# Optimization experiments

Measured on AMD Instinct MI355X. Metric: run time of the kernel, lower is better.

The kernel has to match this reference:

```python
import jax, jax.numpy as jnp
import numpy as np

N, DIM, H, DH = 2048, 1024, 16, 64
LARGE_NEG = -1e10
LN_EPS = 1e-6  # flax LayerNorm default


def setup_inputs() -> dict:
    key = jax.random.key(0)
    ks = jax.random.split(key, 6)
    x = jax.random.normal(ks[0], (N, DIM), dtype=jnp.float32)
    pos_sin = jax.random.uniform(ks[1], (N - 1, DH // 2), dtype=jnp.float32)
    pos_cos = jax.random.uniform(ks[2], (N - 1, DH // 2), dtype=jnp.float32)
    mask = jax.random.bernoulli(ks[3], 0.9, (N - 1,))
    ln_scale = jnp.ones((DIM,), jnp.float32)
    ln_bias = jnp.zeros((DIM,), jnp.float32)
    w_qkv = jax.random.normal(ks[4], (DIM, 3 * H * DH), jnp.float32) * (DIM ** -0.5)
    w_out = jax.random.normal(ks[5], (H * DH, DIM), jnp.float32) * ((H * DH) ** -0.5)
    b_out = jnp.zeros((DIM,), jnp.float32)
    return {"x": x, "pos_sin": pos_sin, "pos_cos": pos_cos, "mask": mask,
            "ln_scale": ln_scale, "ln_bias": ln_bias,
            "w_qkv": w_qkv, "w_out": w_out, "b_out": b_out}


def _rotate_every_two(t):
    # t: [i, h, d] -> pairwise rotation along d
    x1 = t[:, :, ::2]
    x2 = t[:, :, 1::2]
    return jnp.stack((-x2, x1), axis=-1).reshape(t.shape)


def _apply_rope(t, sin, cos):
    # sin/cos: [i, d/2] -> interleave-repeat to [i, 1, d] (einops 'b n -> b (n j)', j=2)
    sin2 = jnp.repeat(sin, 2, axis=-1)[:, None, :]
    cos2 = jnp.repeat(cos, 2, axis=-1)[:, None, :]
    return t * cos2 + _rotate_every_two(t) * sin2


def reference(x, pos_sin, pos_cos, mask, ln_scale, ln_bias, w_qkv, w_out, b_out):
    n, dim_in = x.shape
    scale = dim_in ** -0.5  # NOTE: full model dim, as in the source

    # LayerNorm over last axis
    mu = jnp.mean(x, axis=-1, keepdims=True)
    var = jnp.mean(jnp.square(x - mu), axis=-1, keepdims=True)
    xn = (x - mu) * jax.lax.rsqrt(var + LN_EPS) * ln_scale + ln_bias

    # QKV projection (no bias)
    qkv = xn @ w_qkv  # [n, 3*h*d]
    q, k, v = jnp.split(qkv, 3, axis=-1)
    q, k, v = (t.reshape(n, H, DH) for t in (q, k, v))

    # Selective RoPE: rotate all positions except the first token
    q = q.at[1:].set(_apply_rope(q[1:], pos_sin, pos_cos))
    k = k.at[1:].set(_apply_rope(k[1:], pos_sin, pos_cos))

    # Head-last similarity [i, j, h]
    sim = jnp.einsum('ihd,jhd->ijh', q, k) * scale

    # Padding mask: prepend True for position 0, broadcast as (1, j, 1)
    pad_mask = jnp.pad(mask, (1, 0), constant_values=True)[None, :, None]

    # Causal mask: triu of an (n-1)x(n-1) block padded with False on row/col 0
    tri = jnp.pad(jnp.ones((n - 1, n - 1), bool), ((1, 0), (1, 0)), constant_values=False)
    causal_mask = jnp.triu(tri, 1)[:, :, None]  # k = j - i + 1 = 1
    full_mask = (~causal_mask) & pad_mask

    sim = jnp.where(full_mask, sim, LARGE_NEG)
    attn = jax.nn.softmax(sim, axis=-2)  # softmax over j (non-last axis)

    out = jnp.einsum('ijh,jhd->ihd', attn, v).reshape(n, H * DH)
    return out @ w_out + b_out
```

## Files before the change

### kernel.cpp

```cpp
#include <hip/hip_runtime.h>
#include <hip/hip_bf16.h>
#include <stdint.h>

typedef __bf16 bf16_t;
typedef __bf16 bf16x8 __attribute__((ext_vector_type(8)));
typedef __bf16 bf16x4 __attribute__((ext_vector_type(4)));
typedef float  f32x4  __attribute__((ext_vector_type(4)));

#define DEV __device__ __forceinline__

static constexpr int NTOK = 2048;
static constexpr int DIM  = 1024;
static constexpr int NH   = 16;
static constexpr int DH   = 64;
static constexpr int QKVN = 3072;
static constexpr int SLOTS_PER_HEAD = 40;
static constexpr int PART_SLOTS = 36;
static constexpr int PART_STRIDE = 17408;
static constexpr float L2E = 1.44269504f;

__device__ static constexpr unsigned char SLOT_ORDER[40] = {
    39, 38, 37, 36, 34, 33, 32, 30, 29, 28, 26, 25, 24, 23,
    22, 21, 19, 18, 16, 15, 13, 12, 11, 10, 8, 6, 4, 3,
    35, 20, 9, 2,
    31, 17, 7, 1,
    27, 14, 5, 0};

DEV void gload_lds16(const void* g, void* l) {
  __builtin_amdgcn_global_load_lds(
      (__attribute__((address_space(1))) void*)(g),
      (__attribute__((address_space(3))) void*)(l), 16, 0, 0);
}

DEV float bf2f(bf16_t b) { return (float)b; }

__global__ __launch_bounds__(256) void k_ln_tc(const float* __restrict__ x,
                                               const float* __restrict__ gamma,
                                               const float* __restrict__ beta,
                                               bf16_t* __restrict__ xn,
                                               const float* __restrict__ wsrc,
                                               bf16_t* __restrict__ wdst,
                                               const float* __restrict__ wosrc,
                                               bf16_t* __restrict__ wodst) {
  __shared__ float tile[64][65];
  __shared__ float red[8];
  int b = blockIdx.x;
  if (b < NTOK) {
    const int row = b;
    const int t = threadIdx.x;
    const float4* x4 = reinterpret_cast<const float4*>(x);
    float4 v = x4[(size_t)row * 256 + t];
    float s  = v.x + v.y + v.z + v.w;
    float s2 = v.x * v.x + v.y * v.y + v.z * v.z + v.w * v.w;
#pragma unroll
    for (int o = 1; o < 64; o <<= 1) {
      s  += __shfl_xor(s, o, 64);
      s2 += __shfl_xor(s2, o, 64);
    }
    const int w = t >> 6, lane = t & 63;
    if (lane == 0) { red[w] = s; red[4 + w] = s2; }
    __syncthreads();
    s  = red[0] + red[1] + red[2] + red[3];
    s2 = red[4] + red[5] + red[6] + red[7];
    const float mu  = s * (1.0f / 1024.0f);
    const float var = s2 * (1.0f / 1024.0f) - mu * mu;
    const float inv = rsqrtf(var + 1e-6f);
    const float4 g = reinterpret_cast<const float4*>(gamma)[t];
    const float4 bb = reinterpret_cast<const float4*>(beta)[t];
    bf16x4 o;
    o[0] = (bf16_t)((v.x - mu) * inv * g.x + bb.x);
    o[1] = (bf16_t)((v.y - mu) * inv * g.y + bb.y);
    o[2] = (bf16_t)((v.z - mu) * inv * g.z + bb.z);
    o[3] = (bf16_t)((v.w - mu) * inv * g.w + bb.w);
    *reinterpret_cast<bf16x4*>(xn + (size_t)row * DIM + t * 4) = o;
  } else if (b < NTOK + 768) {
    b -= NTOK;
    const int c0 = (b % 48) * 64;
    const int r0 = (b / 48) * 64;
    const int tx = threadIdx.x & 63;
    const int ty = threadIdx.x >> 6;
#pragma unroll
    for (int i = 0; i < 16; ++i) {
      int r = ty + i * 4;
      tile[r][tx] = wsrc[(size_t)(r0 + r) * 3072 + c0 + tx];
    }
    __syncthreads();
#pragma unroll
    for (int i = 0; i < 16; ++i) {
      int r = ty + i * 4;
      wdst[(size_t)(c0 + r) * 1024 + r0 + tx] = (bf16_t)tile[tx][r];
    }
  } else {
    b -= (NTOK + 768);
    const int c0 = (b & 15) * 64;
    const int r0 = (b >> 4) * 64;
    const int tx = threadIdx.x & 63;
    const int ty = threadIdx.x >> 6;
#pragma unroll
    for (int i = 0; i < 16; ++i) {
      int r = ty + i * 4;
      tile[r][tx] = wosrc[(size_t)(r0 + r) * 1024 + c0 + tx];
    }
    __syncthreads();
#pragma unroll
    for (int i = 0; i < 16; ++i) {
      int r = ty + i * 4;
      wodst[(size_t)(c0 + r) * 1024 + r0 + tx] = (bf16_t)tile[tx][r];
    }
  }
}

__global__ __launch_bounds__(256) void k_gemm_qkv(const bf16_t* __restrict__ A,
                                                  const bf16_t* __restrict__ Bt,
                                                  bf16_t* __restrict__ qkv,
                                                  bf16_t* __restrict__ Vt,
                                                  const float* __restrict__ psin,
                                                  const float* __restrict__ pcos) {
  __shared__ alignas(16) bf16_t As[2][128 * 32];
  __shared__ alignas(16) bf16_t Bs[2][128 * 32];
  const int K = DIM;
  const int tid = threadIdx.x, lane = tid & 63, w = tid >> 6;
  const int bm = blockIdx.x * 128, bn = blockIdx.y * 128;
  const int wr = (w >> 1) * 64, wc = (w & 1) * 64;
  f32x4 acc[4][4];
#pragma unroll
  for (int i = 0; i < 4; ++i)
#pragma unroll
    for (int j = 0; j < 4; ++j) acc[i][j] = f32x4{0.f, 0.f, 0.f, 0.f};

  const int srow  = lane >> 2;
  const int scol8 = (lane & 3) * 8;

#define GSTAGEQ(KT, BUF)                                                              \
  {                                                                                   \
    _Pragma("unroll") for (int it = 0; it < 2; ++it) {                                \
      int seg = w * 2 + it;                                                           \
      gload_lds16(A  + (size_t)(bm + seg * 16 + srow) * K + (KT) + scol8,             \
                  (char*)As + (BUF) * 8192 + seg * 1024 + lane * 16);                 \
      gload_lds16(Bt + (size_t)(bn + seg * 16 + srow) * K + (KT) + scol8,             \
                  (char*)Bs + (BUF) * 8192 + seg * 1024 + lane * 16);                 \
    }                                                                                 \
  }

  GSTAGEQ(0, 0)
  int buf = 0;
  for (int kt = 0; kt < K; kt += 32, buf ^= 1) {
    if (kt + 32 < K) {
      GSTAGEQ(kt + 32, buf ^ 1)
      asm volatile("s_waitcnt vmcnt(4)" ::: "memory");
    } else {
      asm volatile("s_waitcnt vmcnt(0)" ::: "memory");
    }
    __builtin_amdgcn_s_barrier();
    bf16x8 af[4], bfr[4];
#pragma unroll
    for (int i = 0; i < 4; ++i) {
      int mrow = wr + i * 16 + (lane & 15);
      af[i] = *reinterpret_cast<const bf16x8*>((const char*)As + buf * 8192 + mrow * 64 +
                                               (lane >> 4) * 16);
    }
#pragma unroll
    for (int j = 0; j < 4; ++j) {
      int nrow = wc + j * 16 + (lane & 15);
      bfr[j] = *reinterpret_cast<const bf16x8*>((const char*)Bs + buf * 8192 + nrow * 64 +
                                                (lane >> 4) * 16);
    }
#pragma unroll
    for (int i = 0; i < 4; ++i)
#pragma unroll
      for (int j = 0; j < 4; ++j)
        acc[i][j] = __builtin_amdgcn_mfma_f32_16x16x32_bf16(af[i], bfr[j], acc[i][j], 0, 0, 0);
    __builtin_amdgcn_s_barrier();
  }
#undef GSTAGEQ

  if (bn >= 2048) {
#pragma unroll
    for (int i = 0; i < 4; ++i)
#pragma unroll
      for (int j = 0; j < 4; ++j) {
        int d = bn - 2048 + wc + j * 16 + (lane & 15);
        int n0v = bm + wr + i * 16 + (lane >> 4) * 4;
        bf16x4 v4;
#pragma unroll
        for (int r = 0; r < 4; ++r) v4[r] = (bf16_t)acc[i][j][r];
        *reinterpret_cast<bf16x4*>(Vt + (size_t)d * NTOK + n0v) = v4;
      }
  } else {
#pragma unroll
    for (int i = 0; i < 4; ++i)
#pragma unroll
      for (int j = 0; j < 4; ++j) {
        int nn = bn + wc + j * 16 + (lane & 15);
        int tt = (nn & 63) >> 1;
        bool isq = nn < 1024;
#pragma unroll
        for (int r = 0; r < 4; ++r) {
          int mm = bm + wr + i * 16 + (lane >> 4) * 4 + r;
          float v = acc[i][j][r];
          float p = __shfl_xor(v, 1, 64);
          int pidx = (mm >= 1 ? mm - 1 : 0) * 32 + tt;
          float sn = psin[pidx], cs = pcos[pidx];
          float roped = (nn & 1) ? (v * cs + p * sn) : (v * cs - p * sn);
          if (mm < 1) roped = v;
          if (isq && mm >= 1) roped *= 0.03125f;
          qkv[(size_t)mm * QKVN + nn] = (bf16_t)roped;
        }
      }
  }
}

template <int F32OUT>
__global__ __launch_bounds__(256) void k_gemm64(const bf16_t* __restrict__ A,
                                                const bf16_t* __restrict__ Bt,
                                                bf16_t* __restrict__ Cb,
                                                float* __restrict__ Cf,
                                                const float* __restrict__ bias,
                                                int M, int N, int K) {
  __shared__ alignas(16) bf16_t As[2][64 * 32];
  __shared__ alignas(16) bf16_t Bs[2][128 * 32];
  const int tid = threadIdx.x, lane = tid & 63, w = tid >> 6;
  const int bm = blockIdx.x * 64, bn = blockIdx.y * 128;
  const int wr = (w >> 1) * 32, wc = (w & 1) * 64;
  f32x4 acc[2][4];
#pragma unroll
  for (int i = 0; i < 2; ++i)
#pragma unroll
    for (int j = 0; j < 4; ++j) acc[i][j] = f32x4{0.f, 0.f, 0.f, 0.f};

  const int srow  = lane >> 2;
  const int scol8 = (lane & 3) * 8;

#define GSTAGE64(KT, BUF)                                                             \
  {                                                                                   \
    _Pragma("unroll") for (int it = 0; it < 3; ++it) {                                \
      int s = w * 3 + it;                                                             \
      if (s < 4)                                                                      \
        gload_lds16(A + (size_t)(bm + s * 16 + srow) * K + (KT) + scol8,              \
                    (char*)As + (BUF) * 4096 + s * 1024 + lane * 16);                 \
      else                                                                            \
        gload_lds16(Bt + (size_t)(bn + (s - 4) * 16 + srow) * K + (KT) + scol8,       \
                    (char*)Bs + (BUF) * 8192 + (s - 4) * 1024 + lane * 16);           \
    }                                                                                 \
  }

  GSTAGE64(0, 0)
  int buf = 0;
  for (int kt = 0; kt < K; kt += 32, buf ^= 1) {
    if (kt + 32 < K) {
      GSTAGE64(kt + 32, buf ^ 1)
      asm volatile("s_waitcnt vmcnt(3)" ::: "memory");
    } else {
      asm volatile("s_waitcnt vmcnt(0)" ::: "memory");
    }
    __builtin_amdgcn_s_barrier();
    bf16x8 af[2], bfr[4];
#pragma unroll
    for (int i = 0; i < 2; ++i) {
      int mrow = wr + i * 16 + (lane & 15);
      af[i] = *reinterpret_cast<const bf16x8*>((const char*)As + buf * 4096 + mrow * 64 +
                                               (lane >> 4) * 16);
    }
#pragma unroll
    for (int j = 0; j < 4; ++j) {
      int nrow = wc + j * 16 + (lane & 15);
      bfr[j] = *reinterpret_cast<const bf16x8*>((const char*)Bs + buf * 8192 + nrow * 64 +
                                                (lane >> 4) * 16);
    }
#pragma unroll
    for (int i = 0; i < 2; ++i)
#pragma unroll
      for (int j = 0; j < 4; ++j)
        acc[i][j] = __builtin_amdgcn_mfma_f32_16x16x32_bf16(af[i], bfr[j], acc[i][j], 0, 0, 0);
    __builtin_amdgcn_s_barrier();
  }
#undef GSTAGE64

#pragma unroll
  for (int i = 0; i < 2; ++i)
#pragma unroll
    for (int j = 0; j < 4; ++j)
#pragma unroll
      for (int r = 0; r < 4; ++r) {
        int mm = bm + wr + i * 16 + (lane >> 4) * 4 + r;
        int nn = bn + wc + j * 16 + (lane & 15);
        float val = acc[i][j][r];
        if (F32OUT)
          Cf[(size_t)mm * N + nn] = val + bias[nn];
        else
          Cb[(size_t)mm * N + nn] = (bf16_t)val;
      }
}

__global__ __launch_bounds__(512) void k_attn_part(const bf16_t* __restrict__ qkv,
                                                   const bf16_t* __restrict__ Vt,
                                                   const int* __restrict__ mask,
                                                   char* __restrict__ part,
                                                   bf16_t* __restrict__ Ob) {
  __shared__ alignas(16) bf16_t Ks[2][64][64];
  __shared__ alignas(16) bf16_t Vs[2][64][64];
  __shared__ alignas(16) float padf[512];

  const int idx = blockIdx.x;
  const int h = idx & 15;
  const int rank = idx >> 4;

  if (rank == 0) {
    float* qv   = padf;
    float* sbuf = (float*)Ks;
    float* red  = (float*)Vs;
    float* red2 = (float*)Vs + 64;
    const int t = threadIdx.x, lane = t & 63, w8 = t >> 6;
    if (t < 64) qv[t] = (float)qkv[h * DH + t];
    __syncthreads();
    float sm[4];
    float lmax = -1e30f;
#pragma unroll
    for (int p = 0; p < 4; ++p) {
      int j = p * 512 + t;
      const bf16_t* kr = qkv + (size_t)j * QKVN + DIM + h * DH;
      float s = 0.f;
#pragma unroll
      for (int u = 0; u < 8; ++u) {
        bf16x8 kv8 = *reinterpret_cast<const bf16x8*>(kr + u * 8);
#pragma unroll
        for (int e = 0; e < 8; ++e) s += qv[u * 8 + e] * (float)kv8[e];
      }
      bool padj = (j == 0) || (mask[j - 1] != 0);
      s = padj ? s * 0.03125f : -1e30f;
      sm[p] = s;
      lmax = fmaxf(lmax, s);
    }
#pragma unroll
    for (int o = 1; o < 64; o <<= 1) lmax = fmaxf(lmax, __shfl_xor(lmax, o, 64));
    if (lane == 0) red[w8] = lmax;
    __syncthreads();
    float M = red[0];
#pragma unroll
    for (int i = 1; i < 8; ++i) M = fmaxf(M, red[i]);
    __syncthreads();
    float ls = 0.f;
#pragma unroll
    for (int p = 0; p < 4; ++p) {
      float pe = __expf(sm[p] - M);
      sbuf[p * 512 + t] = pe;
      ls += pe;
    }
#pragma unroll
    for (int o = 1; o < 64; o <<= 1) ls += __shfl_xor(ls, o, 64);
    if (lane == 0) red[w8] = ls;
    __syncthreads();
    float L = red[0];
#pragma unroll
    for (int i = 1; i < 8; ++i) L += red[i];

    const int d = t & 63, qr = t >> 6;
    const bf16_t* vr = Vt + ((size_t)h * DH + d) * NTOK + qr * 256;
    float a = 0.f;
#pragma unroll 8
    for (int u = 0; u < 32; ++u) {
      bf16x8 v8 = *reinterpret_cast<const bf16x8*>(vr + u * 8);
#pragma unroll
      for (int e = 0; e < 8; ++e) a += sbuf[qr * 256 + u * 8 + e] * (float)v8[e];
    }
    red2[qr * 64 + d] = a;
    __syncthreads();
    if (t < 64) {
      float o = 0.f;
#pragma unroll
      for (int i = 0; i < 8; ++i) o += red2[i * 64 + t];
      Ob[h * DH + t] = (bf16_t)(o / L);
    }
    return;
  }

  const int slot = SLOT_ORDER[rank - 1];
  int gq;
  if (slot < 4) gq = 0; else if (slot < 12) gq = 1; else if (slot < 24) gq = 2; else gq = 3;
  const int tt = slot - 2 * gq * (gq + 1);
  const int Q = (gq << 2) + tt / (gq + 1);
  const int c2 = tt - (tt / (gq + 1)) * (gq + 1);
  const int q0 = Q * 128;
  const int kbeg = c2 * 512;
  const int kvlen = (Q + 1) * 128;
  const int klen = min(512, kvlen - kbeg);
  const int ntiles = klen >> 6;
  const int nch = gq + 1;

  const int tid = threadIdx.x, lane = tid & 63, w = tid >> 6;
  const int g = lane >> 4;
  const int c = lane & 15;

  for (int jr = tid; jr < klen; jr += 512) {
    int j = kbeg + jr;
    padf[jr] = (j == 0 || mask[j - 1] != 0) ? 1.f : 0.f;
  }

  const int iw = q0 + w * 16;
  bf16x8 qf[2];
  {
    const bf16_t* qp = qkv + (size_t)(iw + c) * QKVN + h * DH + g * 8;
    qf[0] = *reinterpret_cast<const bf16x8*>(qp);
    qf[1] = *reinterpret_cast<const bf16x8*>(qp + 32);
  }
  bf16x8 ones;
#pragma unroll
  for (int e = 0; e < 8; ++e) ones[e] = (bf16_t)1.0f;

  float m_run = -1e30f, m2 = -1e30f;
  f32x4 acc[4], accl;
#pragma unroll
  for (int df = 0; df < 4; ++df) acc[df] = f32x4{0.f, 0.f, 0.f, 0.f};
  accl = f32x4{0.f, 0.f, 0.f, 0.f};

  const int r8 = lane >> 3;

#define STAGE(KB, BUF)                                                                   \
  {                                                                                      \
    _Pragma("unroll") for (int i2 = 0; i2 < 2; ++i2) {                                   \
      int s = w * 2 + i2;                                                                \
      int sw = (lane & 7) ^ r8 ^ ((s & 3) << 1);                                         \
      if (s < 8) {                                                                       \
        int row = s * 8 + r8;                                                            \
        gload_lds16(qkv + (size_t)((KB) + row) * QKVN + DIM + h * DH + sw * 8,           \
                    (char*)Ks + (BUF)*8192 + s * 1024 + lane * 16);                      \
      } else {                                                                           \
        int row = (s - 8) * 8 + r8;                                                      \
        gload_lds16(Vt + ((size_t)h * DH + row) * NTOK + (KB) + sw * 8,                  \
                    (char*)Vs + (BUF)*8192 + (s - 8) * 1024 + lane * 16);                \
      }                                                                                  \
    }                                                                                    \
  }

  STAGE(kbeg, 0)

  for (int it = 0; it < ntiles; ++it) {
    const int buf = it & 1;
    if (it + 1 < ntiles) {
      STAGE(kbeg + (it + 1) * 64, buf ^ 1)
      asm volatile("s_waitcnt vmcnt(2)" ::: "memory");
    } else {
      asm volatile("s_waitcnt vmcnt(0)" ::: "memory");
    }
    __builtin_amdgcn_s_barrier();

    const int k0 = kbeg + it * 64;
    if (k0 <= iw + 15) {
      const char* KsT = (const char*)Ks + buf * 8192;
      const char* VsT = (const char*)Vs + buf * 8192;

      f32x4 sfr[4];
      __builtin_amdgcn_s_setprio(1);
#pragma unroll
      for (int f = 0; f < 4; ++f) {
        int key7 = ((f & 1) * 4) | (c & 3);
        int key = (f >> 1) * 32 + (c >> 2) * 8 + key7;
        int phi = key7 ^ (((c >> 2) & 3) << 1);
        f32x4 s = f32x4{0.f, 0.f, 0.f, 0.f};
#pragma unroll
        for (int kd = 0; kd < 2; ++kd) {
          bf16x8 kf = *reinterpret_cast<const bf16x8*>(
              KsT + key * 128 + (((kd * 4 + g) ^ phi) << 4));
          s = __builtin_amdgcn_mfma_f32_16x16x32_bf16(kf, qf[kd], s, 0, 0, 0);
        }
        sfr[f] = s;
      }
      __builtin_amdgcn_s_setprio(0);

      float pm = fmaxf(fmaxf(sfr[0][0], sfr[0][1]), fmaxf(sfr[0][2], sfr[0][3]));
#pragma unroll
      for (int f = 1; f < 4; ++f)
        pm = fmaxf(pm, fmaxf(fmaxf(sfr[f][0], sfr[f][1]), fmaxf(sfr[f][2], sfr[f][3])));
      pm = fmaxf(pm, __shfl_xor(pm, 16, 64));
      pm = fmaxf(pm, __shfl_xor(pm, 32, 64));

      if (!__all(pm <= m_run + 8.f)) {
        float mnew = fmaxf(m_run, pm);
        float corr = __builtin_amdgcn_exp2f((m_run - mnew) * L2E);
        m_run = mnew;
        m2 = mnew * L2E;
#pragma unroll
        for (int r = 0; r < 4; ++r) {
          float cr = __shfl(corr, g * 4 + r, 64);
          accl[r] *= cr;
#pragma unroll
          for (int df = 0; df < 4; ++df) acc[df][r] *= cr;
        }
      }

      const bool needC = (k0 + 63 > iw);
      const int qlane = iw + c;
      bf16x8 pa[2];
#pragma unroll
      for (int f = 0; f < 4; ++f) {
        int jb = (k0 - kbeg) + (f >> 1) * 32 + g * 8 + (f & 1) * 4;
        f32x4 pad4 = *reinterpret_cast<const f32x4*>(padf + jb);
#pragma unroll
        for (int r = 0; r < 4; ++r) {
          float pe = __builtin_amdgcn_exp2f(__builtin_fmaf(sfr[f][r], L2E, -m2)) * pad4[r];
          if (needC) pe = (kbeg + jb + r <= qlane) ? pe : 0.f;
          pa[f >> 1][(f & 1) * 4 + r] = (bf16_t)pe;
        }
      }

      __builtin_amdgcn_s_setprio(1);
#pragma unroll
      for (int ks = 0; ks < 2; ++ks) {
        accl = __builtin_amdgcn_mfma_f32_16x16x32_bf16(pa[ks], ones, accl, 0, 0, 0);
#pragma unroll
        for (int df = 0; df < 4; ++df) {
          int d = df * 16 + c;
          int phv = (d & 7) ^ (((d >> 3) & 3) << 1);
          bf16x8 vf = *reinterpret_cast<const bf16x8*>(
              VsT + d * 128 + (((ks * 4 + g) ^ phv) << 4));
          acc[df] = __builtin_amdgcn_mfma_f32_16x16x32_bf16(pa[ks], vf, acc[df], 0, 0, 0);
        }
      }
      __builtin_amdgcn_s_setprio(0);
    }
    __builtin_amdgcn_s_barrier();
  }
#undef STAGE

  if (nch == 1) {
#pragma unroll
    for (int r = 0; r < 4; ++r) {
      float inv = 1.0f / accl[r];
      int row = w * 16 + g * 4 + r;
#pragma unroll
      for (int df = 0; df < 4; ++df) {
        if (q0 + row != 0)
          Ob[(size_t)(q0 + row) * DIM + h * DH + df * 16 + c] = (bf16_t)(acc[df][r] * inv);
      }
    }
    return;
  }

  char* pb = part + (size_t)(h * PART_SLOTS + (slot - 4)) * PART_STRIDE;
  bf16_t* po = (bf16_t*)pb;
  float* pmo = (float*)(pb + 16384);
  float* plo = (float*)(pb + 16896);
  float mq[4];
#pragma unroll
  for (int r = 0; r < 4; ++r) mq[r] = __shfl(m2, g * 4 + r, 64);
#pragma unroll
  for (int df = 0; df < 4; ++df)
#pragma unroll
    for (int r = 0; r < 4; ++r) {
      int row = w * 16 + g * 4 + r;
      po[row * 64 + df * 16 + c] = (bf16_t)acc[df][r];
    }
  if (c == 0) {
#pragma unroll
    for (int r = 0; r < 4; ++r) {
      int row = w * 16 + g * 4 + r;
      pmo[row] = mq[r];
      plo[row] = accl[r];
    }
  }
}

__global__ __launch_bounds__(256) void k_merge(const char* __restrict__ part,
                                               bf16_t* __restrict__ Ob) {
  const int Q = blockIdx.x + 4, h = blockIdx.y;
  const int g = Q >> 2, nch = g + 1;
  const int cum = 2 * g * (g + 1) + (Q & 3) * nch - 4;
  const int t = threadIdx.x;
  const int row = t >> 1, half = t & 1;

  float acc[32];
#pragma unroll
  for (int e = 0; e < 32; ++e) acc[e] = 0.f;
  float M = -3e38f, L = 0.f;

  for (int c = 0; c < nch; ++c) {
    const char* pb = part + (size_t)(h * PART_SLOTS + cum + c) * PART_STRIDE;
    float mc = ((const float*)(pb + 16384))[row];
    float lc = ((const float*)(pb + 16896))[row];
    float Mn = fmaxf(M, mc);
    float sOld = __builtin_amdgcn_exp2f(M - Mn), sNew = __builtin_amdgcn_exp2f(mc - Mn);
    M = Mn;
    L = L * sOld + lc * sNew;
    const bf16_t* od = (const bf16_t*)pb + row * 64 + half * 32;
#pragma unroll
    for (int e4 = 0; e4 < 4; ++e4) {
      bf16x8 o8 = *reinterpret_cast<const bf16x8*>(od + e4 * 8);
#pragma unroll
      for (int e = 0; e < 8; ++e)
        acc[e4 * 8 + e] = acc[e4 * 8 + e] * sOld + (float)o8[e] * sNew;
    }
  }
  const float inv = 1.0f / L;
  bf16_t* dst = Ob + (size_t)(Q * 128 + row) * DIM + h * DH + half * 32;
#pragma unroll
  for (int e4 = 0; e4 < 4; ++e4) {
    bf16x8 r8o;
#pragma unroll
    for (int e = 0; e < 8; ++e) r8o[e] = (bf16_t)(acc[e4 * 8 + e] * inv);
    *reinterpret_cast<bf16x8*>(dst + e4 * 8) = r8o;
  }
}

extern "C" void kernel_launch(void* const* d_in, const int* in_sizes, int n_in,
                              void* d_out, int out_size, void* d_ws, size_t ws_size,
                              hipStream_t stream) {
  const float* x       = (const float*)d_in[0];
  const float* pos_sin = (const float*)d_in[1];
  const float* pos_cos = (const float*)d_in[2];
  const int*   mask    = (const int*)d_in[3];
  const float* ln_s    = (const float*)d_in[4];
  const float* ln_b    = (const float*)d_in[5];
  const float* w_qkv   = (const float*)d_in[6];
  const float* w_out   = (const float*)d_in[7];
  const float* b_out   = (const float*)d_in[8];
  float* out = (float*)d_out;

  if (ws_size < 33554432u) return;

  char* ws = (char*)d_ws;
  bf16_t* qkv  = (bf16_t*)(ws + 0);
  bf16_t* Vt   = (bf16_t*)(ws + 12582912);
  bf16_t* Ob   = (bf16_t*)(ws + 16777216);
  bf16_t* Wot  = (bf16_t*)(ws + 20971520);
  bf16_t* xn   = (bf16_t*)(ws + 23068672);
  bf16_t* Wqt  = (bf16_t*)(ws + 27262976);
  char*   part = ws + 23068672;

  k_ln_tc<<<NTOK + 768 + 256, 256, 0, stream>>>(x, ln_s, ln_b, xn, w_qkv, Wqt, w_out, Wot);
  k_gemm_qkv<<<dim3(16, 24), 256, 0, stream>>>(xn, Wqt, qkv, Vt, pos_sin, pos_cos);
  k_attn_part<<<16 * (SLOTS_PER_HEAD + 1), 512, 0, stream>>>(qkv, Vt, mask, part, Ob);
  k_merge<<<dim3(12, 16), 256, 0, stream>>>(part, Ob);
  k_gemm64<1><<<dim3(32, 8), 256, 0, stream>>>(Ob, Wot, nullptr, out, b_out,
                                               NTOK, DIM, DIM);
}
```

Before: 92.17 us.

## Split QKV into separate Q and head-major K buffers; shrink out-proj tile

The QKV GEMM epilogue now writes Q into a compact [N,1024] buffer and K into a head-major [H,N,64] layout instead of one interleaved [N,3072] buffer. This lets the attention kernel load contiguous K rows per head, where it previously used strided loads. Separately, the output projection GEMM tile drops from 64x128 to 64x64, doubling the grid to 512 blocks for better CU occupancy at the cost of more redundant A loads. The K epilogue stores become scattered, and the workspace offsets are repacked.

Measured after the change: 86.33 us (median of 2 runs). 6.3% less time.

```diff
diff --git a/kernel.cpp b/kernel.cpp
--- a/kernel.cpp
+++ b/kernel.cpp
@@ -13,7 +13,6 @@
 static constexpr int DIM  = 1024;
 static constexpr int NH   = 16;
 static constexpr int DH   = 64;
-static constexpr int QKVN = 3072;
 static constexpr int SLOTS_PER_HEAD = 40;
 static constexpr int PART_SLOTS = 36;
 static constexpr int PART_STRIDE = 17408;
@@ -112,7 +111,8 @@
 
 __global__ __launch_bounds__(256) void k_gemm_qkv(const bf16_t* __restrict__ A,
                                                   const bf16_t* __restrict__ Bt,
-                                                  bf16_t* __restrict__ qkv,
+                                                  bf16_t* __restrict__ Qp,
+                                                  bf16_t* __restrict__ Kp,
                                                   bf16_t* __restrict__ Vt,
                                                   const float* __restrict__ psin,
                                                   const float* __restrict__ pcos) {
@@ -204,43 +204,46 @@
           float roped = (nn & 1) ? (v * cs + p * sn) : (v * cs - p * sn);
           if (mm < 1) roped = v;
           if (isq && mm >= 1) roped *= 0.03125f;
-          qkv[(size_t)mm * QKVN + nn] = (bf16_t)roped;
+          if (isq)
+            Qp[(size_t)mm * DIM + nn] = (bf16_t)roped;
+          else {
+            int hh = (nn - 1024) >> 6, dd = nn & 63;
+            Kp[((size_t)hh * NTOK + mm) * DH + dd] = (bf16_t)roped;
+          }
         }
       }
   }
 }
 
-template <int F32OUT>
 __global__ __launch_bounds__(256) void k_gemm64(const bf16_t* __restrict__ A,
                                                 const bf16_t* __restrict__ Bt,
-                                                bf16_t* __restrict__ Cb,
                                                 float* __restrict__ Cf,
                                                 const float* __restrict__ bias,
                                                 int M, int N, int K) {
   __shared__ alignas(16) bf16_t As[2][64 * 32];
-  __shared__ alignas(16) bf16_t Bs[2][128 * 32];
+  __shared__ alignas(16) bf16_t Bs[2][64 * 32];
   const int tid = threadIdx.x, lane = tid & 63, w = tid >> 6;
-  const int bm = blockIdx.x * 64, bn = blockIdx.y * 128;
-  const int wr = (w >> 1) * 32, wc = (w & 1) * 64;
-  f32x4 acc[2][4];
+  const int bm = blockIdx.x * 64, bn = blockIdx.y * 64;
+  const int wr = (w >> 1) * 32, wc = (w & 1) * 32;
+  f32x4 acc[2][2];
 #pragma unroll
   for (int i = 0; i < 2; ++i)
 #pragma unroll
-    for (int j = 0; j < 4; ++j) acc[i][j] = f32x4{0.f, 0.f, 0.f, 0.f};
+    for (int j = 0; j < 2; ++j) acc[i][j] = f32x4{0.f, 0.f, 0.f, 0.f};
 
   const int srow  = lane >> 2;
   const int scol8 = (lane & 3) * 8;
 
 #define GSTAGE64(KT, BUF)                                                             \
   {                                                                                   \
-    _Pragma("unroll") for (int it = 0; it < 3; ++it) {                                \
-      int s = w * 3 + it;                                                             \
+    _Pragma("unroll") for (int it = 0; it < 2; ++it) {                                \
+      int s = w * 2 + it;                                                             \
       if (s < 4)                                                                      \
         gload_lds16(A + (size_t)(bm + s * 16 + srow) * K + (KT) + scol8,              \
                     (char*)As + (BUF) * 4096 + s * 1024 + lane * 16);                 \
       else                                                                            \
         gload_lds16(Bt + (size_t)(bn + (s - 4) * 16 + srow) * K + (KT) + scol8,       \
-                    (char*)Bs + (BUF) * 8192 + (s - 4) * 1024 + lane * 16);           \
+                    (char*)Bs + (BUF) * 4096 + (s - 4) * 1024 + lane * 16);           \
     }                                                                                 \
   }
 
@@ -249,12 +252,12 @@
   for (int kt = 0; kt < K; kt += 32, buf ^= 1) {
     if (kt + 32 < K) {
       GSTAGE64(kt + 32, buf ^ 1)
-      asm volatile("s_waitcnt vmcnt(3)" ::: "memory");
+      asm volatile("s_waitcnt vmcnt(2)" ::: "memory");
     } else {
       asm volatile("s_waitcnt vmcnt(0)" ::: "memory");
     }
     __builtin_amdgcn_s_barrier();
-    bf16x8 af[2], bfr[4];
+    bf16x8 af[2], bfr[2];
 #pragma unroll
     for (int i = 0; i < 2; ++i) {
       int mrow = wr + i * 16 + (lane & 15);
@@ -262,15 +265,15 @@
                                                (lane >> 4) * 16);
     }
 #pragma unroll
-    for (int j = 0; j < 4; ++j) {
+    for (int j = 0; j < 2; ++j) {
       int nrow = wc + j * 16 + (lane & 15);
-      bfr[j] = *reinterpret_cast<const bf16x8*>((const char*)Bs + buf * 8192 + nrow * 64 +
+      bfr[j] = *reinterpret_cast<const bf16x8*>((const char*)Bs + buf * 4096 + nrow * 64 +
                                                 (lane >> 4) * 16);
     }
 #pragma unroll
     for (int i = 0; i < 2; ++i)
 #pragma unroll
-      for (int j = 0; j < 4; ++j)
+      for (int j = 0; j < 2; ++j)
         acc[i][j] = __builtin_amdgcn_mfma_f32_16x16x32_bf16(af[i], bfr[j], acc[i][j], 0, 0, 0);
     __builtin_amdgcn_s_barrier();
   }
@@ -279,20 +282,17 @@
 #pragma unroll
   for (int i = 0; i < 2; ++i)
 #pragma unroll
-    for (int j = 0; j < 4; ++j)
+    for (int j = 0; j < 2; ++j)
 #pragma unroll
       for (int r = 0; r < 4; ++r) {
         int mm = bm + wr + i * 16 + (lane >> 4) * 4 + r;
         int nn = bn + wc + j * 16 + (lane & 15);
-        float val = acc[i][j][r];
-        if (F32OUT)
-          Cf[(size_t)mm * N + nn] = val + bias[nn];
-        else
-          Cb[(size_t)mm * N + nn] = (bf16_t)val;
+        Cf[(size_t)mm * N + nn] = acc[i][j][r] + bias[nn];
       }
 }
 
-__global__ __launch_bounds__(512) void k_attn_part(const bf16_t* __restrict__ qkv,
+__global__ __launch_bounds__(512) void k_attn_part(const bf16_t* __restrict__ Qp,
+                                                   const bf16_t* __restrict__ Kp,
                                                    const bf16_t* __restrict__ Vt,
                                                    const int* __restrict__ mask,
                                                    char* __restrict__ part,
@@ -311,14 +311,14 @@
     float* red  = (float*)Vs;
     float* red2 = (float*)Vs + 64;
     const int t = threadIdx.x, lane = t & 63, w8 = t >> 6;
-    if (t < 64) qv[t] = (float)qkv[h * DH + t];
+    if (t < 64) qv[t] = (float)Qp[h * DH + t];
     __syncthreads();
     float sm[4];
     float lmax = -1e30f;
 #pragma unroll
     for (int p = 0; p < 4; ++p) {
       int j = p * 512 + t;
-      const bf16_t* kr = qkv + (size_t)j * QKVN + DIM + h * DH;
+      const bf16_t* kr = Kp + ((size_t)h * NTOK + j) * DH;
       float s = 0.f;
 #pragma unroll
       for (int u = 0; u < 8; ++u) {
@@ -399,7 +399,7 @@
   const int iw = q0 + w * 16;
   bf16x8 qf[2];
   {
-    const bf16_t* qp = qkv + (size_t)(iw + c) * QKVN + h * DH + g * 8;
+    const bf16_t* qp = Qp + (size_t)(iw + c) * DIM + h * DH + g * 8;
     qf[0] = *reinterpret_cast<const bf16x8*>(qp);
     qf[1] = *reinterpret_cast<const bf16x8*>(qp + 32);
   }
@@ -422,7 +422,7 @@
       int sw = (lane & 7) ^ r8 ^ ((s & 3) << 1);                                         \
       if (s < 8) {                                                                       \
         int row = s * 8 + r8;                                                            \
-        gload_lds16(qkv + (size_t)((KB) + row) * QKVN + DIM + h * DH + sw * 8,           \
+        gload_lds16(Kp + ((size_t)h * NTOK + (KB) + row) * DH + sw * 8,                  \
                     (char*)Ks + (BUF)*8192 + s * 1024 + lane * 16);                      \
       } else {                                                                           \
         int row = (s - 8) * 8 + r8;                                                      \
@@ -618,18 +618,18 @@
   if (ws_size < 33554432u) return;
 
   char* ws = (char*)d_ws;
-  bf16_t* qkv  = (bf16_t*)(ws + 0);
-  bf16_t* Vt   = (bf16_t*)(ws + 12582912);
-  bf16_t* Ob   = (bf16_t*)(ws + 16777216);
-  bf16_t* Wot  = (bf16_t*)(ws + 20971520);
-  bf16_t* xn   = (bf16_t*)(ws + 23068672);
-  bf16_t* Wqt  = (bf16_t*)(ws + 27262976);
-  char*   part = ws + 23068672;
+  bf16_t* Qp   = (bf16_t*)(ws + 0);
+  bf16_t* Kp   = (bf16_t*)(ws + 4194304);
+  bf16_t* Vt   = (bf16_t*)(ws + 8388608);
+  bf16_t* Ob   = (bf16_t*)(ws + 12582912);
+  bf16_t* Wot  = (bf16_t*)(ws + 16777216);
+  bf16_t* xn   = (bf16_t*)(ws + 18874368);
+  bf16_t* Wqt  = (bf16_t*)(ws + 23068672);
+  char*   part = ws + 18874368;
 
   k_ln_tc<<<NTOK + 768 + 256, 256, 0, stream>>>(x, ln_s, ln_b, xn, w_qkv, Wqt, w_out, Wot);
-  k_gemm_qkv<<<dim3(16, 24), 256, 0, stream>>>(xn, Wqt, qkv, Vt, pos_sin, pos_cos);
-  k_attn_part<<<16 * (SLOTS_PER_HEAD + 1), 512, 0, stream>>>(qkv, Vt, mask, part, Ob);
+  k_gemm_qkv<<<dim3(16, 24), 256, 0, stream>>>(xn, Wqt, Qp, Kp, Vt, pos_sin, pos_cos);
+  k_attn_part<<<16 * (SLOTS_PER_HEAD + 1), 512, 0, stream>>>(Qp, Kp, Vt, mask, part, Ob);
   k_merge<<<dim3(12, 16), 256, 0, stream>>>(part, Ob);
-  k_gemm64<1><<<dim3(32, 8), 256, 0, stream>>>(Ob, Wot, nullptr, out, b_out,
-                                               NTOK, DIM, DIM);
+  k_gemm64<<<dim3(32, 16), 256, 0, stream>>>(Ob, Wot, out, b_out, NTOK, DIM, DIM);
 }
```
